# Kernel optimization log

Measured on AMD Instinct MI355X. Metric: run time of the kernel, lower is better.

Reference implementation:

```python
import jax, jax.numpy as jnp
import numpy as np

D_MODEL = 1024
NUM_HEADS = 16
D_K = D_MODEL // NUM_HEADS
LOCAL_WINDOW = 3
STRIDE = 4


def strided_mask(seq_len):
    # position i attends to j iff j <= i and (i-j <= local_window or (i-j) % stride == 0)
    i = jnp.arange(seq_len)[:, None]
    j = jnp.arange(seq_len)[None, :]
    d = i - j
    return (d >= 0) & ((d <= LOCAL_WINDOW) | (d % STRIDE == 0))


def setup_inputs() -> dict:
    key = jax.random.key(0)
    ks = jax.random.split(key, 11)
    B, S, D = 4, 1024, D_MODEL
    s = 1.0 / np.sqrt(D)
    inp = {
        "Q": jax.random.normal(ks[0], (B, S, D), jnp.float32),
        "K": jax.random.normal(ks[1], (B, S, D), jnp.float32),
        "V": jax.random.normal(ks[2], (B, S, D), jnp.float32),
        "Wq": jax.random.normal(ks[3], (D, D), jnp.float32) * s,
        "bq": jnp.zeros((D,), jnp.float32),
        "Wk": jax.random.normal(ks[4], (D, D), jnp.float32) * s,
        "bk": jnp.zeros((D,), jnp.float32),
        "Wv": jax.random.normal(ks[5], (D, D), jnp.float32) * s,
        "bv": jnp.zeros((D,), jnp.float32),
        "Wo": jax.random.normal(ks[6], (D, D), jnp.float32) * s,
        "bo": jnp.zeros((D,), jnp.float32),
    }
    return inp


def reference(Q, K, V, Wq, bq, Wk, bk, Wv, bv, Wo, bo):
    B, S, D = Q.shape
    H, dk = NUM_HEADS, D_K

    def split(x):  # [B,S,D] -> [B,H,S,dk]
        return x.reshape(B, S, H, dk).transpose(0, 2, 1, 3)

    q = split(Q @ Wq + bq)
    k = split(K @ Wk + bk)
    v = split(V @ Wv + bv)

    scores = jnp.einsum("bhsd,bhtd->bhst", q, k) / jnp.sqrt(
        jnp.asarray(dk, jnp.float32))
    m = strided_mask(S)[None, None]  # [1,1,S,S]
    scores = jnp.where(m, scores, -1e9)
    attn = jax.nn.softmax(scores, axis=-1)
    out = jnp.einsum("bhst,bhtd->bhsd", attn, v)
    out = out.transpose(0, 2, 1, 3).reshape(B, S, D)  # combine heads
    return out @ Wo + bo
```

## Files before the change

kernel.cpp:

```cpp
#include <hip/hip_runtime.h>

typedef _Float16 f16;
typedef __attribute__((ext_vector_type(8))) _Float16 f16x8;
typedef __attribute__((ext_vector_type(4))) _Float16 f16x4;
typedef __attribute__((ext_vector_type(4))) float f32x4;

#define MFMA16(a, b, c) __builtin_amdgcn_mfma_f32_16x16x32_f16((a), (b), (c), 0, 0, 0)

__device__ __forceinline__ void gld_lds16(const void* g, void* l) {
  __builtin_amdgcn_global_load_lds(
      (__attribute__((address_space(1))) void*)const_cast<void*>(g),
      (__attribute__((address_space(3))) void*)l, 16, 0, 0);
}

__device__ __forceinline__ f16x8 ld8(const f16* p) { return *(const f16x8*)p; }

__global__ __launch_bounds__(256) void cvt_x_kernel(
    const float* __restrict__ Q, const float* __restrict__ K, const float* __restrict__ V,
    f16* __restrict__ oq, f16* __restrict__ ok, f16* __restrict__ ov) {
  const float* src = blockIdx.z == 0 ? Q : (blockIdx.z == 1 ? K : V);
  f16* dst = blockIdx.z == 0 ? oq : (blockIdx.z == 1 ? ok : ov);
  size_t i = ((size_t)blockIdx.x * 256 + threadIdx.x) * 4;
  float4 f = *(const float4*)(src + i);
  f16x4 o4;
  o4.x = (f16)f.x; o4.y = (f16)f.y; o4.z = (f16)f.z; o4.w = (f16)f.w;
  *(f16x4*)(dst + i) = o4;
}

__global__ __launch_bounds__(256) void cvt_wT_kernel(
    const float* __restrict__ Wq, const float* __restrict__ Wk,
    const float* __restrict__ Wv, const float* __restrict__ Wo,
    f16* __restrict__ Tq, f16* __restrict__ Tk, f16* __restrict__ Tv, f16* __restrict__ To) {
  const int z = blockIdx.z;
  const float* W = z == 0 ? Wq : (z == 1 ? Wk : (z == 2 ? Wv : Wo));
  f16* T = z == 0 ? Tq : (z == 1 ? Tk : (z == 2 ? Tv : To));
  __shared__ float tile[64][65];
  const int k0 = blockIdx.x * 64, n0 = blockIdx.y * 64;
  const int tx = threadIdx.x & 63, ty = threadIdx.x >> 6;
#pragma unroll
  for (int rr = 0; rr < 16; ++rr) {
    int r = rr * 4 + ty;
    tile[r][tx] = W[(size_t)(k0 + r) * 1024 + n0 + tx];
  }
  __syncthreads();
#pragma unroll
  for (int rr = 0; rr < 16; ++rr) {
    int nn = rr * 4 + ty;
    T[(size_t)(n0 + nn) * 1024 + k0 + tx] = (f16)tile[tx][nn];
  }
}

template <bool QKV>
__global__ __launch_bounds__(256) void gemm_bt_kernel(
    const f16* __restrict__ A0, const f16* __restrict__ A1, const f16* __restrict__ A2,
    const f16* __restrict__ B0, const f16* __restrict__ B1, const f16* __restrict__ B2,
    const float* __restrict__ bias0, const float* __restrict__ bias1, const float* __restrict__ bias2,
    f16* __restrict__ C0, f16* __restrict__ C1, f16* __restrict__ C2,
    f16* __restrict__ C3, float* __restrict__ Cf) {
  const int z = blockIdx.z;
  const f16* A = z == 0 ? A0 : (z == 1 ? A1 : A2);
  const f16* Bt = z == 0 ? B0 : (z == 1 ? B1 : B2);
  const float* bias = z == 0 ? bias0 : (z == 1 ? bias1 : bias2);

  __shared__ alignas(16) f16 lA[128 * 32];
  __shared__ alignas(16) f16 lB[128 * 32];

  const int t = threadIdx.x;
  const int w = t >> 6, lane = t & 63, quad = lane >> 4, l15 = lane & 15;
  const int wm = w >> 1, wn = w & 1;
  const int mbase = blockIdx.x * 128;
  const int nbase = blockIdx.y * 128;

  const f32x4 zero4 = {0.f, 0.f, 0.f, 0.f};
  f32x4 acc[4][4];
#pragma unroll
  for (int mi = 0; mi < 4; ++mi)
#pragma unroll
    for (int ni = 0; ni < 4; ++ni) acc[mi][ni] = zero4;

  const int r = t >> 2;
  const int koff = (t & 3) * 8;

  for (int k0 = 0; k0 < 1024; k0 += 32) {
    __syncthreads();
    gld_lds16(A + (size_t)(mbase + r) * 1024 + k0 + koff, (char*)lA + w * 1024);
    gld_lds16(A + (size_t)(mbase + 64 + r) * 1024 + k0 + koff, (char*)lA + 4096 + w * 1024);
    gld_lds16(Bt + (size_t)(nbase + r) * 1024 + k0 + koff, (char*)lB + w * 1024);
    gld_lds16(Bt + (size_t)(nbase + 64 + r) * 1024 + k0 + koff, (char*)lB + 4096 + w * 1024);
    __syncthreads();

    f16x8 af[4], bf[4];
#pragma unroll
    for (int mi = 0; mi < 4; ++mi)
      af[mi] = ld8(&lA[(wm * 64 + mi * 16 + l15) * 32 + quad * 8]);
#pragma unroll
    for (int ni = 0; ni < 4; ++ni)
      bf[ni] = ld8(&lB[(wn * 64 + ni * 16 + l15) * 32 + quad * 8]);
#pragma unroll
    for (int mi = 0; mi < 4; ++mi)
#pragma unroll
      for (int ni = 0; ni < 4; ++ni)
        acc[mi][ni] = MFMA16(af[mi], bf[ni], acc[mi][ni]);
  }

#pragma unroll
  for (int mi = 0; mi < 4; ++mi) {
#pragma unroll
    for (int ni = 0; ni < 4; ++ni) {
#pragma unroll
      for (int rg = 0; rg < 4; ++rg) {
        const int row = mbase + wm * 64 + mi * 16 + quad * 4 + rg;
        const int col = nbase + wn * 64 + ni * 16 + l15;
        const float v = acc[mi][ni][rg] + bias[col];
        if (QKV) {
          const int bh = (row >> 10) * 16 + (col >> 6);
          const int s = row & 1023, d = col & 63;
          const f16 hv = (f16)v;
          if (z != 2) {
            f16* Ch = (z == 0) ? C0 : C1;
            Ch[(size_t)bh * 65536 + s * 64 + d] = hv;
          } else {
            C2[(size_t)bh * 65536 + s * 64 + d] = hv;
            const int rr = s & 3, n = s >> 2, wi = n & 63;
            C3[(size_t)bh * 65536 + (size_t)rr * 16384 + (size_t)d * 256 +
               (n & ~63) + ((wi & 15) << 2) + (wi >> 4)] = hv;
          }
        } else {
          Cf[(size_t)row * 1024 + col] = v;
        }
      }
    }
  }
}

__global__ __launch_bounds__(256) void gemm_out_kernel(
    const f16* __restrict__ A, const f16* __restrict__ Bt,
    const float* __restrict__ bias, float* __restrict__ Cf) {
  __shared__ alignas(16) f16 lA[64 * 32];
  __shared__ alignas(16) f16 lB[128 * 32];

  const int t = threadIdx.x;
  const int w = t >> 6, lane = t & 63, quad = lane >> 4, l15 = lane & 15;
  const int wm = w >> 1, wn = w & 1;
  const int mbase = blockIdx.x * 64;
  const int nbase = blockIdx.y * 128;

  const f32x4 zero4 = {0.f, 0.f, 0.f, 0.f};
  f32x4 acc[2][4];
#pragma unroll
  for (int mi = 0; mi < 2; ++mi)
#pragma unroll
    for (int ni = 0; ni < 4; ++ni) acc[mi][ni] = zero4;

  const int r = t >> 2;
  const int koff = (t & 3) * 8;

  for (int k0 = 0; k0 < 1024; k0 += 32) {
    __syncthreads();
    gld_lds16(A + (size_t)(mbase + r) * 1024 + k0 + koff, (char*)lA + w * 1024);
    gld_lds16(Bt + (size_t)(nbase + r) * 1024 + k0 + koff, (char*)lB + w * 1024);
    gld_lds16(Bt + (size_t)(nbase + 64 + r) * 1024 + k0 + koff, (char*)lB + 4096 + w * 1024);
    __syncthreads();

    f16x8 af[2], bf[4];
#pragma unroll
    for (int mi = 0; mi < 2; ++mi)
      af[mi] = ld8(&lA[(wm * 32 + mi * 16 + l15) * 32 + quad * 8]);
#pragma unroll
    for (int ni = 0; ni < 4; ++ni)
      bf[ni] = ld8(&lB[(wn * 64 + ni * 16 + l15) * 32 + quad * 8]);
#pragma unroll
    for (int mi = 0; mi < 2; ++mi)
#pragma unroll
      for (int ni = 0; ni < 4; ++ni)
        acc[mi][ni] = MFMA16(af[mi], bf[ni], acc[mi][ni]);
  }

#pragma unroll
  for (int mi = 0; mi < 2; ++mi)
#pragma unroll
    for (int ni = 0; ni < 4; ++ni)
#pragma unroll
      for (int rg = 0; rg < 4; ++rg) {
        const int row = mbase + wm * 32 + mi * 16 + quad * 4 + rg;
        const int col = nbase + wn * 64 + ni * 16 + l15;
        Cf[(size_t)row * 1024 + col] = acc[mi][ni][rg] + bias[col];
      }
}

__global__ __launch_bounds__(256) void attn_far_kernel(
    const f16* __restrict__ qh, const f16* __restrict__ kh,
    const f16* __restrict__ vtg, float* __restrict__ po, float* __restrict__ ml) {
  const int t = threadIdx.x;
  const int w = t >> 6, lane = t & 63, quad = lane >> 4, l15 = lane & 15;
  const int widx = blockIdx.x + 512 * w;
  const int bh = (widx & 255) >> 2, r = widx & 3;
  const int wq = widx >> 8;
  const int m0 = wq * 32;
  const int ntiles = (wq >> 1) + 1;

  __shared__ alignas(16) f16 lp[4][2][16 * 72];

  const f16* qb = qh + (size_t)bh * 65536;
  const f16* kb = kh + (size_t)bh * 65536;
  const f16* vb = vtg + (size_t)bh * 65536 + (size_t)r * 16384;
  const float SCL2 = 0.125f * 1.44269504f;

  f16x8 aq[2][2];
#pragma unroll
  for (int mt = 0; mt < 2; ++mt) {
    const int i = 4 * (m0 + mt * 16 + l15) + r;
#pragma unroll
    for (int ko = 0; ko < 2; ++ko)
      aq[mt][ko] = ld8(qb + (size_t)i * 64 + ko * 32 + quad * 8);
  }

  const f32x4 zero4 = {0.f, 0.f, 0.f, 0.f};
  f32x4 o[2][4];
  float mrun[2][4], lrun[2][4];
#pragma unroll
  for (int mt = 0; mt < 2; ++mt)
#pragma unroll
    for (int i = 0; i < 4; ++i) {
      o[mt][i] = zero4; mrun[mt][i] = -1e30f; lrun[mt][i] = 0.f;
    }

  for (int jt = 0; jt < ntiles; ++jt) {
    const int n0 = jt * 64;
    f16x8 bk0[4], bk1[4], bv0[4], bv1[4];
#pragma unroll
    for (int nt = 0; nt < 4; ++nt) {
      const f16* kr = kb + (size_t)(4 * (n0 + nt * 16 + l15) + r) * 64;
      bk0[nt] = ld8(kr + quad * 8);
      bk1[nt] = ld8(kr + 32 + quad * 8);
      const f16* vr = vb + (size_t)(nt * 16 + l15) * 256 + n0;
      bv0[nt] = ld8(vr + quad * 8);
      bv1[nt] = ld8(vr + 32 + quad * 8);
    }
    const bool lastt = (jt == ntiles - 1);
#pragma unroll
    for (int mt = 0; mt < 2; ++mt) {
      f32x4 sc[4];
#pragma unroll
      for (int nt = 0; nt < 4; ++nt) {
        f32x4 c = MFMA16(aq[mt][0], bk0[nt], zero4);
        sc[nt] = MFMA16(aq[mt][1], bk1[nt], c);
      }
#pragma unroll
      for (int rg = 0; rg < 4; ++rg) {
        const int m = m0 + mt * 16 + quad * 4 + rg;
        float s[4];
#pragma unroll
        for (int nt = 0; nt < 4; ++nt) {
          float vsc = sc[nt][rg] * SCL2;
          if (lastt) vsc = (n0 + nt * 16 + l15 < m) ? vsc : -3.0e38f;
          s[nt] = vsc;
        }
        float tm = fmaxf(fmaxf(s[0], s[1]), fmaxf(s[2], s[3]));
        tm = fmaxf(tm, __shfl_xor(tm, 1));
        tm = fmaxf(tm, __shfl_xor(tm, 2));
        tm = fmaxf(tm, __shfl_xor(tm, 4));
        tm = fmaxf(tm, __shfl_xor(tm, 8));
        const float mnew = fmaxf(mrun[mt][rg], tm);
        const float alpha = exp2f(mrun[mt][rg] - mnew);
        float p[4], ps = 0.f;
#pragma unroll
        for (int nt = 0; nt < 4; ++nt) { p[nt] = exp2f(s[nt] - mnew); ps += p[nt]; }
        ps += __shfl_xor(ps, 1);
        ps += __shfl_xor(ps, 2);
        ps += __shfl_xor(ps, 4);
        ps += __shfl_xor(ps, 8);
        lrun[mt][rg] = lrun[mt][rg] * alpha + ps;
        mrun[mt][rg] = mnew;
#pragma unroll
        for (int ntv = 0; ntv < 4; ++ntv) o[mt][ntv][rg] *= alpha;
        f16x4 pk;
        pk.x = (f16)p[0]; pk.y = (f16)p[1]; pk.z = (f16)p[2]; pk.w = (f16)p[3];
        *(f16x4*)&lp[w][mt][(quad * 4 + rg) * 72 + l15 * 4] = pk;
      }
    }
#pragma unroll
    for (int mt = 0; mt < 2; ++mt) {
      const f16x8 ap0 = ld8(&lp[w][mt][l15 * 72 + quad * 8]);
      const f16x8 ap1 = ld8(&lp[w][mt][l15 * 72 + 32 + quad * 8]);
#pragma unroll
      for (int ntv = 0; ntv < 4; ++ntv) {
        f32x4 c = MFMA16(ap0, bv0[ntv], o[mt][ntv]);
        o[mt][ntv] = MFMA16(ap1, bv1[ntv], c);
      }
    }
  }

#pragma unroll
  for (int mt = 0; mt < 2; ++mt)
#pragma unroll
    for (int rg = 0; rg < 4; ++rg) {
      const int i = 4 * (m0 + mt * 16 + quad * 4 + rg) + r;
      const size_t idx = (size_t)bh * 1024 + i;
#pragma unroll
      for (int ntv = 0; ntv < 4; ++ntv)
        po[idx * 64 + ntv * 16 + l15] = o[mt][ntv][rg];
      if (l15 == 0) { ml[idx * 2] = mrun[mt][rg]; ml[idx * 2 + 1] = lrun[mt][rg]; }
    }
}

__global__ __launch_bounds__(256) void attn_diag_kernel(
    const f16* __restrict__ qh, const f16* __restrict__ kh, const f16* __restrict__ vh,
    const float* __restrict__ po, const float* __restrict__ ml, f16* __restrict__ ao) {
  const int t = threadIdx.x;
  const int widx = blockIdx.x * 4 + (t >> 6);
  const int l = t & 63;
  const int bh = widx >> 10, i = widx & 1023;
  const float SCL2 = 0.125f * 1.44269504f;

  const float q = (float)qh[(size_t)bh * 65536 + (size_t)i * 64 + l];
  float s[4];
#pragma unroll
  for (int d = 0; d < 4; ++d) {
    const int j = i - d;
    const int jc = j < 0 ? 0 : j;
    float pr = q * (float)kh[(size_t)bh * 65536 + (size_t)jc * 64 + l];
    pr += __shfl_xor(pr, 1);
    pr += __shfl_xor(pr, 2);
    pr += __shfl_xor(pr, 4);
    pr += __shfl_xor(pr, 8);
    pr += __shfl_xor(pr, 16);
    pr += __shfl_xor(pr, 32);
    s[d] = (j >= 0) ? pr * SCL2 : -3.0e38f;
  }
  const float md = fmaxf(fmaxf(s[0], s[1]), fmaxf(s[2], s[3]));
  const size_t idx = (size_t)bh * 1024 + i;
  const float mf = ml[idx * 2], lf = ml[idx * 2 + 1];
  const float M = fmaxf(md, mf);
  float p[4], ld = 0.f;
#pragma unroll
  for (int d = 0; d < 4; ++d) { p[d] = exp2f(s[d] - M); ld += p[d]; }
  float ov = 0.f;
#pragma unroll
  for (int d = 0; d < 4; ++d) {
    const int jc = (i - d) < 0 ? 0 : (i - d);
    ov += p[d] * (float)vh[(size_t)bh * 65536 + (size_t)jc * 64 + l];
  }
  const float fs = exp2f(mf - M);
  const float lt = lf * fs + ld;
  const float of = po[idx * 64 + l];
  const float res = (of * fs + ov) / lt;
  const int b = bh >> 4, h = bh & 15;
  ao[((size_t)(b * 1024 + i)) * 1024 + h * 64 + l] = (f16)res;
}

extern "C" void kernel_launch(void* const* d_in, const int* in_sizes, int n_in,
                              void* d_out, int out_size, void* d_ws, size_t ws_size,
                              hipStream_t stream) {
  const float* Q = (const float*)d_in[0];
  const float* K = (const float*)d_in[1];
  const float* V = (const float*)d_in[2];
  const float* Wq = (const float*)d_in[3];
  const float* bq = (const float*)d_in[4];
  const float* Wk = (const float*)d_in[5];
  const float* bk = (const float*)d_in[6];
  const float* Wv = (const float*)d_in[7];
  const float* bv = (const float*)d_in[8];
  const float* Wo = (const float*)d_in[9];
  const float* bo = (const float*)d_in[10];
  float* out = (float*)d_out;

  char* ws = (char*)d_ws;
  const size_t MB = 1ull << 20;
  f16* Xq  = (f16*)(ws + 0 * MB);
  f16* Xk  = (f16*)(ws + 8 * MB);
  f16* Xv  = (f16*)(ws + 16 * MB);
  f16* TWq = (f16*)(ws + 24 * MB);
  f16* TWk = (f16*)(ws + 26 * MB);
  f16* TWv = (f16*)(ws + 28 * MB);
  f16* TWo = (f16*)(ws + 30 * MB);
  f16* qhb = (f16*)(ws + 32 * MB);
  f16* khb = (f16*)(ws + 40 * MB);
  f16* vhb = (f16*)(ws + 48 * MB);
  f16* vtg = (f16*)(ws + 56 * MB);
  float* po  = (float*)(ws + 0 * MB);
  float* mlb = (float*)(ws + 16 * MB);
  f16* aob   = (f16*)(ws + 17 * MB);

  cvt_x_kernel<<<dim3(4096, 1, 3), 256, 0, stream>>>(Q, K, V, Xq, Xk, Xv);
  cvt_wT_kernel<<<dim3(16, 16, 4), 256, 0, stream>>>(Wq, Wk, Wv, Wo, TWq, TWk, TWv, TWo);
  gemm_bt_kernel<true><<<dim3(32, 8, 3), 256, 0, stream>>>(
      Xq, Xk, Xv, TWq, TWk, TWv, bq, bk, bv, qhb, khb, vhb, vtg, nullptr);
  attn_far_kernel<<<dim3(512), 256, 0, stream>>>(qhb, khb, vtg, po, mlb);
  attn_diag_kernel<<<dim3(16384), 256, 0, stream>>>(qhb, khb, vhb, po, mlb, aob);
  gemm_out_kernel<<<dim3(64, 8), 256, 0, stream>>>(aob, TWo, bo, out);
}
```

Measured before the change: 228.3 us.

## Merge conversion kernels, move diagonal into far pass, vectorize diag kernel

Merges the activation cast and weight-transpose kernels into one launch, removing a kernel launch. The far-attention kernel now covers the d=0 diagonal term via its mask, so the diag kernel handles only offsets 1..3. The diag kernel is rewritten so each lane owns 8 contiguous dims of one row, using 16-byte vector loads and stores and a 3-step shuffle reduction, with 8x fewer blocks. In exchange, 3/4 of the blocks in the merged z=3 slice exit immediately.

```diff
diff --git a/kernel.cpp b/kernel.cpp
--- a/kernel.cpp
+++ b/kernel.cpp
@@ -15,27 +15,29 @@
 
 __device__ __forceinline__ f16x8 ld8(const f16* p) { return *(const f16x8*)p; }
 
-__global__ __launch_bounds__(256) void cvt_x_kernel(
+__global__ __launch_bounds__(256) void cvt_all_kernel(
     const float* __restrict__ Q, const float* __restrict__ K, const float* __restrict__ V,
-    f16* __restrict__ oq, f16* __restrict__ ok, f16* __restrict__ ov) {
-  const float* src = blockIdx.z == 0 ? Q : (blockIdx.z == 1 ? K : V);
-  f16* dst = blockIdx.z == 0 ? oq : (blockIdx.z == 1 ? ok : ov);
-  size_t i = ((size_t)blockIdx.x * 256 + threadIdx.x) * 4;
-  float4 f = *(const float4*)(src + i);
-  f16x4 o4;
-  o4.x = (f16)f.x; o4.y = (f16)f.y; o4.z = (f16)f.z; o4.w = (f16)f.w;
-  *(f16x4*)(dst + i) = o4;
-}
-
-__global__ __launch_bounds__(256) void cvt_wT_kernel(
+    f16* __restrict__ oq, f16* __restrict__ ok, f16* __restrict__ ov,
     const float* __restrict__ Wq, const float* __restrict__ Wk,
     const float* __restrict__ Wv, const float* __restrict__ Wo,
     f16* __restrict__ Tq, f16* __restrict__ Tk, f16* __restrict__ Tv, f16* __restrict__ To) {
-  const int z = blockIdx.z;
-  const float* W = z == 0 ? Wq : (z == 1 ? Wk : (z == 2 ? Wv : Wo));
-  f16* T = z == 0 ? Tq : (z == 1 ? Tk : (z == 2 ? Tv : To));
   __shared__ float tile[64][65];
-  const int k0 = blockIdx.x * 64, n0 = blockIdx.y * 64;
+  if (blockIdx.z < 3) {
+    const float* src = blockIdx.z == 0 ? Q : (blockIdx.z == 1 ? K : V);
+    f16* dst = blockIdx.z == 0 ? oq : (blockIdx.z == 1 ? ok : ov);
+    size_t i = ((size_t)blockIdx.x * 256 + threadIdx.x) * 4;
+    float4 f = *(const float4*)(src + i);
+    f16x4 o4;
+    o4.x = (f16)f.x; o4.y = (f16)f.y; o4.z = (f16)f.z; o4.w = (f16)f.w;
+    *(f16x4*)(dst + i) = o4;
+    return;
+  }
+  if (blockIdx.x >= 1024) return;
+  const int zz = blockIdx.x >> 8;
+  const float* W = zz == 0 ? Wq : (zz == 1 ? Wk : (zz == 2 ? Wv : Wo));
+  f16* T = zz == 0 ? Tq : (zz == 1 ? Tk : (zz == 2 ? Tv : To));
+  const int tidx = blockIdx.x & 255;
+  const int k0 = (tidx & 15) * 64, n0 = (tidx >> 4) * 64;
   const int tx = threadIdx.x & 63, ty = threadIdx.x >> 6;
 #pragma unroll
   for (int rr = 0; rr < 16; ++rr) {
@@ -253,7 +255,7 @@
 #pragma unroll
         for (int nt = 0; nt < 4; ++nt) {
           float vsc = sc[nt][rg] * SCL2;
-          if (lastt) vsc = (n0 + nt * 16 + l15 < m) ? vsc : -3.0e38f;
+          if (lastt) vsc = (n0 + nt * 16 + l15 <= m) ? vsc : -3.0e38f;
           s[nt] = vsc;
         }
         float tm = fmaxf(fmaxf(s[0], s[1]), fmaxf(s[2], s[3]));
@@ -308,45 +310,57 @@
     const f16* __restrict__ qh, const f16* __restrict__ kh, const f16* __restrict__ vh,
     const float* __restrict__ po, const float* __restrict__ ml, f16* __restrict__ ao) {
   const int t = threadIdx.x;
-  const int widx = blockIdx.x * 4 + (t >> 6);
-  const int l = t & 63;
-  const int bh = widx >> 10, i = widx & 1023;
+  const int w = t >> 6, lane = t & 63;
+  const int ri = lane >> 3, c8 = lane & 7;
+  const int g = blockIdx.x * 4 + w;
+  const int bh = g >> 7;
+  const int i = ((g & 127) << 3) + ri;
   const float SCL2 = 0.125f * 1.44269504f;
 
-  const float q = (float)qh[(size_t)bh * 65536 + (size_t)i * 64 + l];
-  float s[4];
-#pragma unroll
-  for (int d = 0; d < 4; ++d) {
+  const size_t rb = (size_t)bh * 65536;
+  const f16x8 q8 = ld8(qh + rb + (size_t)i * 64 + c8 * 8);
+  float qf[8];
+#pragma unroll
+  for (int e = 0; e < 8; ++e) qf[e] = (float)q8[e];
+
+  float s[3];
+  f16x8 v8[3];
+#pragma unroll
+  for (int d = 1; d <= 3; ++d) {
     const int j = i - d;
     const int jc = j < 0 ? 0 : j;
-    float pr = q * (float)kh[(size_t)bh * 65536 + (size_t)jc * 64 + l];
+    const f16x8 k8 = ld8(kh + rb + (size_t)jc * 64 + c8 * 8);
+    v8[d - 1] = ld8(vh + rb + (size_t)jc * 64 + c8 * 8);
+    float pr = 0.f;
+#pragma unroll
+    for (int e = 0; e < 8; ++e) pr = fmaf(qf[e], (float)k8[e], pr);
     pr += __shfl_xor(pr, 1);
     pr += __shfl_xor(pr, 2);
     pr += __shfl_xor(pr, 4);
-    pr += __shfl_xor(pr, 8);
-    pr += __shfl_xor(pr, 16);
-    pr += __shfl_xor(pr, 32);
-    s[d] = (j >= 0) ? pr * SCL2 : -3.0e38f;
-  }
-  const float md = fmaxf(fmaxf(s[0], s[1]), fmaxf(s[2], s[3]));
+    s[d - 1] = (j >= 0) ? pr * SCL2 : -3.0e38f;
+  }
+  const float md = fmaxf(fmaxf(s[0], s[1]), s[2]);
   const size_t idx = (size_t)bh * 1024 + i;
-  const float mf = ml[idx * 2], lf = ml[idx * 2 + 1];
+  const float2 mlv = *(const float2*)(ml + idx * 2);
+  const float mf = mlv.x, lf = mlv.y;
   const float M = fmaxf(md, mf);
-  float p[4], ld = 0.f;
-#pragma unroll
-  for (int d = 0; d < 4; ++d) { p[d] = exp2f(s[d] - M); ld += p[d]; }
-  float ov = 0.f;
-#pragma unroll
-  for (int d = 0; d < 4; ++d) {
-    const int jc = (i - d) < 0 ? 0 : (i - d);
-    ov += p[d] * (float)vh[(size_t)bh * 65536 + (size_t)jc * 64 + l];
-  }
+  float p[3], ld = 0.f;
+#pragma unroll
+  for (int d = 0; d < 3; ++d) { p[d] = exp2f(s[d] - M); ld += p[d]; }
   const float fs = exp2f(mf - M);
-  const float lt = lf * fs + ld;
-  const float of = po[idx * 64 + l];
-  const float res = (of * fs + ov) / lt;
+  const float inv = 1.0f / (lf * fs + ld);
+  const float4 po0 = *(const float4*)(po + idx * 64 + c8 * 8);
+  const float4 po1 = *(const float4*)(po + idx * 64 + c8 * 8 + 4);
+  float pe[8] = {po0.x, po0.y, po0.z, po0.w, po1.x, po1.y, po1.z, po1.w};
+  f16x8 r8;
+#pragma unroll
+  for (int e = 0; e < 8; ++e) {
+    const float ov = p[0] * (float)v8[0][e] + p[1] * (float)v8[1][e] +
+                     p[2] * (float)v8[2][e];
+    r8[e] = (f16)((pe[e] * fs + ov) * inv);
+  }
   const int b = bh >> 4, h = bh & 15;
-  ao[((size_t)(b * 1024 + i)) * 1024 + h * 64 + l] = (f16)res;
+  *(f16x8*)(ao + ((size_t)(b * 1024 + i)) * 1024 + h * 64 + c8 * 8) = r8;
 }
 
 extern "C" void kernel_launch(void* const* d_in, const int* in_sizes, int n_in,
@@ -382,11 +396,11 @@
   float* mlb = (float*)(ws + 16 * MB);
   f16* aob   = (f16*)(ws + 17 * MB);
 
-  cvt_x_kernel<<<dim3(4096, 1, 3), 256, 0, stream>>>(Q, K, V, Xq, Xk, Xv);
-  cvt_wT_kernel<<<dim3(16, 16, 4), 256, 0, stream>>>(Wq, Wk, Wv, Wo, TWq, TWk, TWv, TWo);
+  cvt_all_kernel<<<dim3(4096, 1, 4), 256, 0, stream>>>(
+      Q, K, V, Xq, Xk, Xv, Wq, Wk, Wv, Wo, TWq, TWk, TWv, TWo);
   gemm_bt_kernel<true><<<dim3(32, 8, 3), 256, 0, stream>>>(
       Xq, Xk, Xv, TWq, TWk, TWv, bq, bk, bv, qhb, khb, vhb, vtg, nullptr);
   attn_far_kernel<<<dim3(512), 256, 0, stream>>>(qhb, khb, vtg, po, mlb);
-  attn_diag_kernel<<<dim3(16384), 256, 0, stream>>>(qhb, khb, vhb, po, mlb, aob);
+  attn_diag_kernel<<<dim3(2048), 256, 0, stream>>>(qhb, khb, vhb, po, mlb, aob);
   gemm_out_kernel<<<dim3(64, 8), 256, 0, stream>>>(aob, TWo, bo, out);
 }
```

Result: faster. 215.0 us (-5.8%).
